# Optimization experiments

Measured on AMD Instinct MI355X. Metric: run time of the kernel, lower is better.

The kernel has to match this reference:

```python
import jax, jax.numpy as jnp
import numpy as np

EMB = 512
HEADS = 8
HEAD_DIM = EMB // HEADS


def setup_inputs() -> dict:
    key = jax.random.key(0)
    ks = jax.random.split(key, 6)
    b, t = 2, 4096
    x = jax.random.normal(ks[0], (b, t, EMB), dtype=jnp.float32)
    sc = 1.0 / np.sqrt(HEAD_DIM).astype(np.float32)
    Wq = jax.random.normal(ks[1], (HEAD_DIM, HEAD_DIM), dtype=jnp.float32) * sc
    Wk = jax.random.normal(ks[2], (HEAD_DIM, HEAD_DIM), dtype=jnp.float32) * sc
    Wv = jax.random.normal(ks[3], (HEAD_DIM, HEAD_DIM), dtype=jnp.float32) * sc
    Wu = jax.random.normal(ks[4], (EMB, EMB), dtype=jnp.float32) * (1.0 / np.sqrt(EMB).astype(np.float32))
    bu = jnp.zeros((EMB,), dtype=jnp.float32)
    return {"x": x, "Wq": Wq, "Wk": Wk, "Wv": Wv, "Wu": Wu, "bu": bu}


def reference(x, Wq, Wk, Wv, Wu, bu):
    b, t, e = x.shape
    s = Wq.shape[0]
    h = e // s
    xh = x.reshape(b, t, h, s)
    # torch Linear: y = x @ W.T (no bias for q/k/v)
    q = jnp.einsum('bthd,ed->bthe', xh, Wq)  # e here == s (head dim)
    k = jnp.einsum('bthd,ed->bthe', xh, Wk)
    v = jnp.einsum('bthd,ed->bthe', xh, Wv)
    # full [b,h,t,t] score matrix, scaled by sqrt(emb_dim) as in source
    dot = jnp.einsum('bqhd,bkhd->bhqk', q, k) / (e ** 0.5)
    att = jax.nn.softmax(dot, axis=-1)
    out = jnp.einsum('bhqk,bkhd->bqhd', att, v).reshape(b, t, e)
    return out @ Wu.T + bu
```

## Files before the change

### kernel.cpp

```cpp
#include <hip/hip_runtime.h>
#include <hip/hip_bf16.h>


#define T 4096
#define HEADS 8
#define HD 64
#define EMB 512
#define BATCH 2
#define BH (BATCH * HEADS)

typedef __attribute__((ext_vector_type(8))) short short8;
typedef __attribute__((ext_vector_type(4))) float floatx4;

__device__ inline short f2bf(float f) {
  union { float f; unsigned u; } v; v.f = f;
  unsigned r = v.u + 0x7FFF + ((v.u >> 16) & 1);
  return (short)(r >> 16);
}

__device__ inline short8 pack8(float4 a, float4 b) {
  short8 o;
  o[0] = f2bf(a.x); o[1] = f2bf(a.y); o[2] = f2bf(a.z); o[3] = f2bf(a.w);
  o[4] = f2bf(b.x); o[5] = f2bf(b.y); o[6] = f2bf(b.z); o[7] = f2bf(b.w);
  return o;
}

__device__ inline short8 packbf(float p0, float p1, float p2, float p3,
                                float p4, float p5, float p6, float p7) {
  union { __hip_bfloat162 h[4]; short8 s; } u;
  float2 t;
  t.x = p0; t.y = p1; u.h[0] = __float22bfloat162_rn(t);
  t.x = p2; t.y = p3; u.h[1] = __float22bfloat162_rn(t);
  t.x = p4; t.y = p5; u.h[2] = __float22bfloat162_rn(t);
  t.x = p6; t.y = p7; u.h[3] = __float22bfloat162_rn(t);
  return u.s;
}

__device__ inline int swz(int row, int byte) {
  return (row * 128 + byte) ^ ((row & 7) << 4);
}

__global__ __launch_bounds__(256) void qkv_kernel(
    const float* __restrict__ x, const float* __restrict__ Wq,
    const float* __restrict__ Wk, const float* __restrict__ Wv,
    short* __restrict__ q_ws, short* __restrict__ k_ws, short* __restrict__ vt_ws) {
  __shared__ __align__(16) short xs[256 * 64];
  const int tid = threadIdx.x;
  const int lane = tid & 63;
  const int w = tid >> 6;
  const int g = lane >> 4, lr = lane & 15;
  const long rowbase = (long)blockIdx.x * 256;

  {
    const float4* xv = (const float4*)(x + (rowbase + tid) * 64);
    for (int c = 0; c < 8; ++c) {
      float4 a = xv[2 * c], b = xv[2 * c + 1];
      *(short8*)((char*)xs + swz(tid, c * 16)) = pack8(a, b);
    }
  }
  __syncthreads();

  const float* Ws[3] = {Wq, Wk, Wv};
  for (int m = 0; m < 3; ++m) {
    const float* W = Ws[m];
    for (int nt = 0; nt < 4; ++nt) {
      const int coln = nt * 16 + lr;
      const float4* wr0 = (const float4*)(W + coln * 64 + 8 * g);
      const float4* wr1 = (const float4*)(W + coln * 64 + 32 + 8 * g);
      short8 b0 = pack8(wr0[0], wr0[1]);
      short8 b1 = pack8(wr1[0], wr1[1]);
      for (int mr = 0; mr < 4; ++mr) {
        const int arow = w * 64 + mr * 16 + lr;
        short8 a0 = *(short8*)((char*)xs + swz(arow, g * 16));
        short8 a1 = *(short8*)((char*)xs + swz(arow, 64 + g * 16));
        floatx4 acc = 0;
        acc = __builtin_amdgcn_mfma_f32_16x16x32_bf16(a0, b0, acc, 0, 0, 0);
        acc = __builtin_amdgcn_mfma_f32_16x16x32_bf16(a1, b1, acc, 0, 0, 0);
        for (int jj = 0; jj < 4; ++jj) {
          long R = rowbase + w * 64 + mr * 16 + 4 * g + jj;
          int bb = (int)(R >> 15);
          int h = (int)(R & 7);
          int t = (int)((R >> 3) & 4095);
          if (m == 0)
            q_ws[(((long)(bb * HEADS + h) * T + t) * 64) + coln] = f2bf(acc[jj]);
          else if (m == 1)
            k_ws[(((long)(bb * HEADS + h) * T + t) * 64) + coln] = f2bf(acc[jj]);
          else {
            int tp = (t & ~31) | (((t >> 2) & 3) << 3) | (((t >> 4) & 1) << 2) | (t & 3);
            vt_ws[((long)(bb * HEADS + h) * 64 + coln) * T + tp] = f2bf(acc[jj]);
          }
        }
      }
    }
  }
}

__global__ __launch_bounds__(256) void attn_kernel(
    const short* __restrict__ q_ws, const short* __restrict__ k_ws,
    const short* __restrict__ vt_ws, short* __restrict__ o_ws) {
  __shared__ __align__(16) short Ks[2][64 * 64];
  __shared__ __align__(16) short Vs[2][64 * 64];
  const int tid = threadIdx.x, lane = tid & 63, w = tid >> 6;
  const int g = lane >> 4, lr = lane & 15;
  const int bh = blockIdx.y;
  const int q0 = blockIdx.x * 128;
  const short* Qp = q_ws + (long)bh * T * 64;
  const short* Kp = k_ws + (long)bh * T * 64;
  const short* Vt = vt_ws + (long)bh * 64 * T;

  const float c2 = 0.0441941738241592f * 1.4426950408889634f;

  short8 aq[2][2];
#pragma unroll
  for (int mt = 0; mt < 2; ++mt) {
    int r = q0 + w * 32 + mt * 16 + lr;
    aq[mt][0] = *(const short8*)(Qp + (long)r * 64 + g * 8);
    aq[mt][1] = *(const short8*)(Qp + (long)r * 64 + 32 + g * 8);
  }

  floatx4 acc[2][4];
#pragma unroll
  for (int mt = 0; mt < 2; ++mt)
#pragma unroll
    for (int dt = 0; dt < 4; ++dt) acc[mt][dt] = 0;
  float ellp[2] = {0.f, 0.f};

  const int srow = tid >> 2;
  const int sseg = (tid & 3) * 16;

  {
    const short8* ksrc = (const short8*)(Kp + (long)srow * 64 + sseg);
    short8 k0 = ksrc[0], k1 = ksrc[1];
    const short8* vsrc = (const short8*)(Vt + (long)srow * T + sseg);
    short8 v0 = vsrc[0], v1 = vsrc[1];
    *(short8*)((char*)Ks[0] + swz(srow, sseg * 2)) = k0;
    *(short8*)((char*)Ks[0] + swz(srow, sseg * 2 + 16)) = k1;
    *(short8*)((char*)Vs[0] + swz(srow, sseg * 2)) = v0;
    *(short8*)((char*)Vs[0] + swz(srow, sseg * 2 + 16)) = v1;
  }
  __syncthreads();

  for (int it = 0; it < T / 64; ++it) {
    const int cur = it & 1;
    const int nk = ((it + 1) & (T / 64 - 1)) * 64;
    const short8* ksrc = (const short8*)(Kp + (long)(nk + srow) * 64 + sseg);
    short8 nk0 = ksrc[0], nk1 = ksrc[1];
    const short8* vsrc = (const short8*)(Vt + (long)srow * T + nk + sseg);
    short8 nv0 = vsrc[0], nv1 = vsrc[1];

    char* KsB = (char*)Ks[cur];
    char* VsB = (char*)Vs[cur];

    short8 kb[4][2], vb[4][2];
#pragma unroll
    for (int kt = 0; kt < 4; ++kt) {
      kb[kt][0] = *(short8*)(KsB + swz(kt * 16 + lr, g * 16));
      kb[kt][1] = *(short8*)(KsB + swz(kt * 16 + lr, 64 + g * 16));
    }
#pragma unroll
    for (int dt = 0; dt < 4; ++dt) {
      vb[dt][0] = *(short8*)(VsB + swz(dt * 16 + lr, g * 16));
      vb[dt][1] = *(short8*)(VsB + swz(dt * 16 + lr, 64 + g * 16));
    }

#pragma unroll
    for (int mt = 0; mt < 2; ++mt) {
      floatx4 s[4];
#pragma unroll
      for (int kt = 0; kt < 4; ++kt) {
        floatx4 z = 0;
        z = __builtin_amdgcn_mfma_f32_16x16x32_bf16(kb[kt][0], aq[mt][0], z, 0, 0, 0);
        z = __builtin_amdgcn_mfma_f32_16x16x32_bf16(kb[kt][1], aq[mt][1], z, 0, 0, 0);
        s[kt] = z;
      }
      float p[16];
#pragma unroll
      for (int kt = 0; kt < 4; ++kt) {
#pragma unroll
        for (int r = 0; r < 4; ++r)
          p[kt * 4 + r] = __builtin_amdgcn_exp2f(fmaf(s[kt][r], c2, -3.0f));
      }
#pragma unroll
      for (int e = 0; e < 16; ++e) ellp[mt] += p[e];
      short8 pa0 = packbf(p[0], p[1], p[2], p[3], p[4], p[5], p[6], p[7]);
      short8 pa1 = packbf(p[8], p[9], p[10], p[11], p[12], p[13], p[14], p[15]);
#pragma unroll
      for (int dt = 0; dt < 4; ++dt) {
        acc[mt][dt] = __builtin_amdgcn_mfma_f32_16x16x32_bf16(pa0, vb[dt][0], acc[mt][dt], 0, 0, 0);
        acc[mt][dt] = __builtin_amdgcn_mfma_f32_16x16x32_bf16(pa1, vb[dt][1], acc[mt][dt], 0, 0, 0);
      }
    }

    char* KsN = (char*)Ks[cur ^ 1];
    char* VsN = (char*)Vs[cur ^ 1];
    *(short8*)(KsN + swz(srow, sseg * 2)) = nk0;
    *(short8*)(KsN + swz(srow, sseg * 2 + 16)) = nk1;
    *(short8*)(VsN + swz(srow, sseg * 2)) = nv0;
    *(short8*)(VsN + swz(srow, sseg * 2 + 16)) = nv1;
    __syncthreads();
  }

  float ef[2];
#pragma unroll
  for (int mt = 0; mt < 2; ++mt) {
    float e = ellp[mt];
    e += __shfl_xor(e, 16);
    e += __shfl_xor(e, 32);
    ef[mt] = e;
  }
  const int bb = bh >> 3, h = bh & 7;
#pragma unroll
  for (int mt = 0; mt < 2; ++mt) {
#pragma unroll
    for (int j = 0; j < 4; ++j) {
      float rl = 1.0f / __shfl(ef[mt], 4 * g + j);
      int trow = q0 + w * 32 + mt * 16 + 4 * g + j;
      long ob = ((long)(bb * T + trow)) * EMB + h * 64;
#pragma unroll
      for (int dt = 0; dt < 4; ++dt)
        o_ws[ob + dt * 16 + lr] = f2bf(acc[mt][dt][j] * rl);
    }
  }
}

__global__ __launch_bounds__(256) void proj_kernel(
    const short* __restrict__ o_ws, const float* __restrict__ Wu,
    const float* __restrict__ bu, float* __restrict__ out) {
  __shared__ __align__(16) short As[64 * 64];
  __shared__ __align__(16) short Bs[64 * 64];
  const int tid = threadIdx.x;
  const int lane = tid & 63, w = tid >> 6;
  const int g = lane >> 4, lr = lane & 15;
  const int m0 = blockIdx.x * 64;
  const int n0 = blockIdx.y * 64;

  floatx4 acc[4];
  for (int nt = 0; nt < 4; ++nt) acc[nt] = 0;

  for (int kc = 0; kc < EMB; kc += 64) {
    {
      int row = tid >> 2, kp = (tid & 3) * 16;
      const short8* src = (const short8*)(o_ws + (long)(m0 + row) * EMB + kc + kp);
      short8 v0 = src[0], v1 = src[1];
      *(short8*)((char*)As + swz(row, kp * 2)) = v0;
      *(short8*)((char*)As + swz(row, kp * 2 + 16)) = v1;
    }
    {
      int n = tid >> 2, kp = (tid & 3) * 16;
      const float4* src = (const float4*)(Wu + (long)(n0 + n) * EMB + kc + kp);
      *(short8*)((char*)Bs + swz(n, kp * 2)) = pack8(src[0], src[1]);
      *(short8*)((char*)Bs + swz(n, kp * 2 + 16)) = pack8(src[2], src[3]);
    }
    __syncthreads();

    int arow = w * 16 + lr;
    short8 a0 = *(short8*)((char*)As + swz(arow, g * 16));
    short8 a1 = *(short8*)((char*)As + swz(arow, 64 + g * 16));
    for (int nt = 0; nt < 4; ++nt) {
      int n = nt * 16 + lr;
      short8 b0 = *(short8*)((char*)Bs + swz(n, g * 16));
      short8 b1 = *(short8*)((char*)Bs + swz(n, 64 + g * 16));
      acc[nt] = __builtin_amdgcn_mfma_f32_16x16x32_bf16(a0, b0, acc[nt], 0, 0, 0);
      acc[nt] = __builtin_amdgcn_mfma_f32_16x16x32_bf16(a1, b1, acc[nt], 0, 0, 0);
    }
    __syncthreads();
  }

  for (int nt = 0; nt < 4; ++nt) {
    float bias = bu[n0 + nt * 16 + lr];
    for (int j = 0; j < 4; ++j) {
      int mrow = m0 + w * 16 + 4 * g + j;
      out[(long)mrow * EMB + n0 + nt * 16 + lr] = acc[nt][j] + bias;
    }
  }
}

extern "C" void kernel_launch(void* const* d_in, const int* in_sizes, int n_in,
                              void* d_out, int out_size, void* d_ws, size_t ws_size,
                              hipStream_t stream) {
  const float* x  = (const float*)d_in[0];
  const float* Wq = (const float*)d_in[1];
  const float* Wk = (const float*)d_in[2];
  const float* Wv = (const float*)d_in[3];
  const float* Wu = (const float*)d_in[4];
  const float* bu = (const float*)d_in[5];
  float* out = (float*)d_out;

  const long per = (long)BH * T * 64;
  short* q_ws  = (short*)d_ws;
  short* k_ws  = q_ws + per;
  short* vt_ws = k_ws + per;
  short* o_ws  = vt_ws + per;

  qkv_kernel<<<256, 256, 0, stream>>>(x, Wq, Wk, Wv, q_ws, k_ws, vt_ws);
  attn_kernel<<<dim3(T / 128, BH), 256, 0, stream>>>(q_ws, k_ws, vt_ws, o_ws);
  proj_kernel<<<dim3(BATCH * T / 64, EMB / 64), 256, 0, stream>>>(o_ws, Wu, bu, out);
}
```

Baseline: 132.2 us.

## Software-pipeline attention loop so PV MFMAs overlap next tile's QK and softmax

```diff
diff --git a/kernel.cpp b/kernel.cpp
--- a/kernel.cpp
+++ b/kernel.cpp
@@ -8,6 +8,7 @@
 #define EMB 512
 #define BATCH 2
 #define BH (BATCH * HEADS)
+#define NT (T / 64)
 
 typedef __attribute__((ext_vector_type(8))) short short8;
 typedef __attribute__((ext_vector_type(4))) float floatx4;
@@ -25,14 +26,13 @@
   return o;
 }
 
-__device__ inline short8 packbf(float p0, float p1, float p2, float p3,
-                                float p4, float p5, float p6, float p7) {
+__device__ inline short8 packbf(const float* p) {
   union { __hip_bfloat162 h[4]; short8 s; } u;
   float2 t;
-  t.x = p0; t.y = p1; u.h[0] = __float22bfloat162_rn(t);
-  t.x = p2; t.y = p3; u.h[1] = __float22bfloat162_rn(t);
-  t.x = p4; t.y = p5; u.h[2] = __float22bfloat162_rn(t);
-  t.x = p6; t.y = p7; u.h[3] = __float22bfloat162_rn(t);
+  t.x = p[0]; t.y = p[1]; u.h[0] = __float22bfloat162_rn(t);
+  t.x = p[2]; t.y = p[3]; u.h[1] = __float22bfloat162_rn(t);
+  t.x = p[4]; t.y = p[5]; u.h[2] = __float22bfloat162_rn(t);
+  t.x = p[6]; t.y = p[7]; u.h[3] = __float22bfloat162_rn(t);
   return u.s;
 }
 
@@ -95,6 +95,56 @@
   }
 }
 
+__device__ __forceinline__ void frag_loads(const char* KsB, const char* VsB,
+    int lr, int g, short8 kb[4][2], short8 vb[4][2]) {
+#pragma unroll
+  for (int kt = 0; kt < 4; ++kt) {
+    kb[kt][0] = *(const short8*)(KsB + swz(kt * 16 + lr, g * 16));
+    kb[kt][1] = *(const short8*)(KsB + swz(kt * 16 + lr, 64 + g * 16));
+  }
+#pragma unroll
+  for (int dt = 0; dt < 4; ++dt) {
+    vb[dt][0] = *(const short8*)(VsB + swz(dt * 16 + lr, g * 16));
+    vb[dt][1] = *(const short8*)(VsB + swz(dt * 16 + lr, 64 + g * 16));
+  }
+}
+
+__device__ __forceinline__ void qkt_softmax(const short8 kb[4][2],
+    const short8 aq[2][2], float c2, float ellp[2], short8 pa[2][2]) {
+#pragma unroll
+  for (int mt = 0; mt < 2; ++mt) {
+    floatx4 s[4];
+#pragma unroll
+    for (int kt = 0; kt < 4; ++kt) {
+      floatx4 z = 0;
+      z = __builtin_amdgcn_mfma_f32_16x16x32_bf16(kb[kt][0], aq[mt][0], z, 0, 0, 0);
+      z = __builtin_amdgcn_mfma_f32_16x16x32_bf16(kb[kt][1], aq[mt][1], z, 0, 0, 0);
+      s[kt] = z;
+    }
+    float p[16];
+#pragma unroll
+    for (int kt = 0; kt < 4; ++kt)
+#pragma unroll
+      for (int r = 0; r < 4; ++r)
+        p[kt * 4 + r] = __builtin_amdgcn_exp2f(fmaf(s[kt][r], c2, -3.0f));
+#pragma unroll
+    for (int e = 0; e < 16; ++e) ellp[mt] += p[e];
+    pa[mt][0] = packbf(p);
+    pa[mt][1] = packbf(p + 8);
+  }
+}
+
+__device__ __forceinline__ void do_pv(const short8 pa[2][2],
+    const short8 vb[4][2], floatx4 acc[2][4]) {
+#pragma unroll
+  for (int mt = 0; mt < 2; ++mt)
+#pragma unroll
+    for (int dt = 0; dt < 4; ++dt) {
+      acc[mt][dt] = __builtin_amdgcn_mfma_f32_16x16x32_bf16(pa[mt][0], vb[dt][0], acc[mt][dt], 0, 0, 0);
+      acc[mt][dt] = __builtin_amdgcn_mfma_f32_16x16x32_bf16(pa[mt][1], vb[dt][1], acc[mt][dt], 0, 0, 0);
+    }
+}
+
 __global__ __launch_bounds__(256) void attn_kernel(
     const short* __restrict__ q_ws, const short* __restrict__ k_ws,
     const short* __restrict__ vt_ws, short* __restrict__ o_ws) {
@@ -128,6 +178,8 @@
   const int srow = tid >> 2;
   const int sseg = (tid & 3) * 16;
 
+  short8 paA[2][2], paB[2][2], vbA[4][2], vbB[4][2];
+
   {
     const short8* ksrc = (const short8*)(Kp + (long)srow * 64 + sseg);
     short8 k0 = ksrc[0], k1 = ksrc[1];
@@ -140,65 +192,36 @@
   }
   __syncthreads();
 
-  for (int it = 0; it < T / 64; ++it) {
-    const int cur = it & 1;
-    const int nk = ((it + 1) & (T / 64 - 1)) * 64;
-    const short8* ksrc = (const short8*)(Kp + (long)(nk + srow) * 64 + sseg);
-    short8 nk0 = ksrc[0], nk1 = ksrc[1];
-    const short8* vsrc = (const short8*)(Vt + (long)srow * T + nk + sseg);
-    short8 nv0 = vsrc[0], nv1 = vsrc[1];
-
-    char* KsB = (char*)Ks[cur];
-    char* VsB = (char*)Vs[cur];
-
-    short8 kb[4][2], vb[4][2];
-#pragma unroll
-    for (int kt = 0; kt < 4; ++kt) {
-      kb[kt][0] = *(short8*)(KsB + swz(kt * 16 + lr, g * 16));
-      kb[kt][1] = *(short8*)(KsB + swz(kt * 16 + lr, 64 + g * 16));
-    }
-#pragma unroll
-    for (int dt = 0; dt < 4; ++dt) {
-      vb[dt][0] = *(short8*)(VsB + swz(dt * 16 + lr, g * 16));
-      vb[dt][1] = *(short8*)(VsB + swz(dt * 16 + lr, 64 + g * 16));
-    }
-
-#pragma unroll
-    for (int mt = 0; mt < 2; ++mt) {
-      floatx4 s[4];
-#pragma unroll
-      for (int kt = 0; kt < 4; ++kt) {
-        floatx4 z = 0;
-        z = __builtin_amdgcn_mfma_f32_16x16x32_bf16(kb[kt][0], aq[mt][0], z, 0, 0, 0);
-        z = __builtin_amdgcn_mfma_f32_16x16x32_bf16(kb[kt][1], aq[mt][1], z, 0, 0, 0);
-        s[kt] = z;
-      }
-      float p[16];
-#pragma unroll
-      for (int kt = 0; kt < 4; ++kt) {
-#pragma unroll
-        for (int r = 0; r < 4; ++r)
-          p[kt * 4 + r] = __builtin_amdgcn_exp2f(fmaf(s[kt][r], c2, -3.0f));
-      }
-#pragma unroll
-      for (int e = 0; e < 16; ++e) ellp[mt] += p[e];
-      short8 pa0 = packbf(p[0], p[1], p[2], p[3], p[4], p[5], p[6], p[7]);
-      short8 pa1 = packbf(p[8], p[9], p[10], p[11], p[12], p[13], p[14], p[15]);
-#pragma unroll
-      for (int dt = 0; dt < 4; ++dt) {
-        acc[mt][dt] = __builtin_amdgcn_mfma_f32_16x16x32_bf16(pa0, vb[dt][0], acc[mt][dt], 0, 0, 0);
-        acc[mt][dt] = __builtin_amdgcn_mfma_f32_16x16x32_bf16(pa1, vb[dt][1], acc[mt][dt], 0, 0, 0);
-      }
-    }
-
-    char* KsN = (char*)Ks[cur ^ 1];
-    char* VsN = (char*)Vs[cur ^ 1];
-    *(short8*)(KsN + swz(srow, sseg * 2)) = nk0;
-    *(short8*)(KsN + swz(srow, sseg * 2 + 16)) = nk1;
-    *(short8*)(VsN + swz(srow, sseg * 2)) = nv0;
-    *(short8*)(VsN + swz(srow, sseg * 2 + 16)) = nv1;
-    __syncthreads();
-  }
+#define BODY(IT, paP, vbP, paO, vbO, DO_PV)                                     \
+  {                                                                             \
+    const int nk = (((IT) + 1) & (NT - 1)) * 64;                                \
+    const short8* ksrc = (const short8*)(Kp + (long)(nk + srow) * 64 + sseg);   \
+    short8 nk0 = ksrc[0], nk1 = ksrc[1];                                        \
+    const short8* vsrc = (const short8*)(Vt + (long)srow * T + nk + sseg);      \
+    short8 nv0 = vsrc[0], nv1 = vsrc[1];                                        \
+    const char* KsB = (const char*)Ks[(IT) & 1];                                \
+    const char* VsB = (const char*)Vs[(IT) & 1];                                \
+    short8 kb[4][2];                                                            \
+    frag_loads(KsB, VsB, lr, g, kb, vbO);                                       \
+    qkt_softmax(kb, aq, c2, ellp, paO);                                         \
+    if (DO_PV) do_pv(paP, vbP, acc);                                            \
+    char* KsN = (char*)Ks[((IT) + 1) & 1];                                      \
+    char* VsN = (char*)Vs[((IT) + 1) & 1];                                      \
+    *(short8*)(KsN + swz(srow, sseg * 2)) = nk0;                                \
+    *(short8*)(KsN + swz(srow, sseg * 2 + 16)) = nk1;                           \
+    *(short8*)(VsN + swz(srow, sseg * 2)) = nv0;                                \
+    *(short8*)(VsN + swz(srow, sseg * 2 + 16)) = nv1;                           \
+    __syncthreads();                                                            \
+  }
+
+  BODY(0, paB, vbB, paA, vbA, 0)
+  for (int k = 0; k < NT / 2 - 1; ++k) {
+    BODY(2 * k + 1, paA, vbA, paB, vbB, 1)
+    BODY(2 * k + 2, paB, vbB, paA, vbA, 1)
+  }
+  BODY(NT - 1, paA, vbA, paB, vbB, 1)
+  do_pv(paB, vbB, acc);
+#undef BODY
 
   float ef[2];
 #pragma unroll
```

New measurement: 139.5 us. 5.5% more time.

## Fold softmax scale into Wq, offset into MFMA init, row sums via MFMA

Applied to the files above, without the earlier changes.

```diff
diff --git a/kernel.cpp b/kernel.cpp
--- a/kernel.cpp
+++ b/kernel.cpp
@@ -8,6 +8,7 @@
 #define EMB 512
 #define BATCH 2
 #define BH (BATCH * HEADS)
+#define NT (T / 64)
 
 typedef __attribute__((ext_vector_type(8))) short short8;
 typedef __attribute__((ext_vector_type(4))) float floatx4;
@@ -25,14 +26,13 @@
   return o;
 }
 
-__device__ inline short8 packbf(float p0, float p1, float p2, float p3,
-                                float p4, float p5, float p6, float p7) {
+__device__ inline short8 packbf(const float* p) {
   union { __hip_bfloat162 h[4]; short8 s; } u;
   float2 t;
-  t.x = p0; t.y = p1; u.h[0] = __float22bfloat162_rn(t);
-  t.x = p2; t.y = p3; u.h[1] = __float22bfloat162_rn(t);
-  t.x = p4; t.y = p5; u.h[2] = __float22bfloat162_rn(t);
-  t.x = p6; t.y = p7; u.h[3] = __float22bfloat162_rn(t);
+  t.x = p[0]; t.y = p[1]; u.h[0] = __float22bfloat162_rn(t);
+  t.x = p[2]; t.y = p[3]; u.h[1] = __float22bfloat162_rn(t);
+  t.x = p[4]; t.y = p[5]; u.h[2] = __float22bfloat162_rn(t);
+  t.x = p[6]; t.y = p[7]; u.h[3] = __float22bfloat162_rn(t);
   return u.s;
 }
 
@@ -50,6 +50,7 @@
   const int w = tid >> 6;
   const int g = lane >> 4, lr = lane & 15;
   const long rowbase = (long)blockIdx.x * 256;
+  const float c2 = 0.0441941738241592f * 1.4426950408889634f;
 
   {
     const float4* xv = (const float4*)(x + (rowbase + tid) * 64);
@@ -63,12 +64,18 @@
   const float* Ws[3] = {Wq, Wk, Wv};
   for (int m = 0; m < 3; ++m) {
     const float* W = Ws[m];
+    const float sc = (m == 0) ? c2 : 1.0f;
     for (int nt = 0; nt < 4; ++nt) {
       const int coln = nt * 16 + lr;
       const float4* wr0 = (const float4*)(W + coln * 64 + 8 * g);
       const float4* wr1 = (const float4*)(W + coln * 64 + 32 + 8 * g);
-      short8 b0 = pack8(wr0[0], wr0[1]);
-      short8 b1 = pack8(wr1[0], wr1[1]);
+      float4 w0 = wr0[0], w1 = wr0[1], w2 = wr1[0], w3 = wr1[1];
+      w0.x *= sc; w0.y *= sc; w0.z *= sc; w0.w *= sc;
+      w1.x *= sc; w1.y *= sc; w1.z *= sc; w1.w *= sc;
+      w2.x *= sc; w2.y *= sc; w2.z *= sc; w2.w *= sc;
+      w3.x *= sc; w3.y *= sc; w3.z *= sc; w3.w *= sc;
+      short8 b0 = pack8(w0, w1);
+      short8 b1 = pack8(w2, w3);
       for (int mr = 0; mr < 4; ++mr) {
         const int arow = w * 64 + mr * 16 + lr;
         short8 a0 = *(short8*)((char*)xs + swz(arow, g * 16));
@@ -108,8 +115,6 @@
   const short* Kp = k_ws + (long)bh * T * 64;
   const short* Vt = vt_ws + (long)bh * 64 * T;
 
-  const float c2 = 0.0441941738241592f * 1.4426950408889634f;
-
   short8 aq[2][2];
 #pragma unroll
   for (int mt = 0; mt < 2; ++mt) {
@@ -118,12 +123,18 @@
     aq[mt][1] = *(const short8*)(Qp + (long)r * 64 + 32 + g * 8);
   }
 
+  short8 one8;
+#pragma unroll
+  for (int e = 0; e < 8; ++e) one8[e] = (short)0x3F80;
+
   floatx4 acc[2][4];
-#pragma unroll
-  for (int mt = 0; mt < 2; ++mt)
+  floatx4 acc_ell[2];
+#pragma unroll
+  for (int mt = 0; mt < 2; ++mt) {
+    acc_ell[mt] = 0;
 #pragma unroll
     for (int dt = 0; dt < 4; ++dt) acc[mt][dt] = 0;
-  float ellp[2] = {0.f, 0.f};
+  }
 
   const int srow = tid >> 2;
   const int sseg = (tid & 3) * 16;
@@ -140,55 +151,58 @@
   }
   __syncthreads();
 
-  for (int it = 0; it < T / 64; ++it) {
+  for (int it = 0; it < NT; ++it) {
     const int cur = it & 1;
-    const int nk = ((it + 1) & (T / 64 - 1)) * 64;
+    const int nk = ((it + 1) & (NT - 1)) * 64;
     const short8* ksrc = (const short8*)(Kp + (long)(nk + srow) * 64 + sseg);
     short8 nk0 = ksrc[0], nk1 = ksrc[1];
     const short8* vsrc = (const short8*)(Vt + (long)srow * T + nk + sseg);
     short8 nv0 = vsrc[0], nv1 = vsrc[1];
 
-    char* KsB = (char*)Ks[cur];
-    char* VsB = (char*)Vs[cur];
+    const char* KsB = (const char*)Ks[cur];
+    const char* VsB = (const char*)Vs[cur];
 
     short8 kb[4][2], vb[4][2];
 #pragma unroll
     for (int kt = 0; kt < 4; ++kt) {
-      kb[kt][0] = *(short8*)(KsB + swz(kt * 16 + lr, g * 16));
-      kb[kt][1] = *(short8*)(KsB + swz(kt * 16 + lr, 64 + g * 16));
+      kb[kt][0] = *(const short8*)(KsB + swz(kt * 16 + lr, g * 16));
+      kb[kt][1] = *(const short8*)(KsB + swz(kt * 16 + lr, 64 + g * 16));
     }
 #pragma unroll
     for (int dt = 0; dt < 4; ++dt) {
-      vb[dt][0] = *(short8*)(VsB + swz(dt * 16 + lr, g * 16));
-      vb[dt][1] = *(short8*)(VsB + swz(dt * 16 + lr, 64 + g * 16));
+      vb[dt][0] = *(const short8*)(VsB + swz(dt * 16 + lr, g * 16));
+      vb[dt][1] = *(const short8*)(VsB + swz(dt * 16 + lr, 64 + g * 16));
     }
 
 #pragma unroll
     for (int mt = 0; mt < 2; ++mt) {
       floatx4 s[4];
+      __builtin_amdgcn_s_setprio(1);
 #pragma unroll
       for (int kt = 0; kt < 4; ++kt) {
-        floatx4 z = 0;
+        floatx4 z = {-3.f, -3.f, -3.f, -3.f};
         z = __builtin_amdgcn_mfma_f32_16x16x32_bf16(kb[kt][0], aq[mt][0], z, 0, 0, 0);
         z = __builtin_amdgcn_mfma_f32_16x16x32_bf16(kb[kt][1], aq[mt][1], z, 0, 0, 0);
         s[kt] = z;
       }
+      __builtin_amdgcn_s_setprio(0);
       float p[16];
 #pragma unroll
-      for (int kt = 0; kt < 4; ++kt) {
+      for (int kt = 0; kt < 4; ++kt)
 #pragma unroll
         for (int r = 0; r < 4; ++r)
-          p[kt * 4 + r] = __builtin_amdgcn_exp2f(fmaf(s[kt][r], c2, -3.0f));
-      }
-#pragma unroll
-      for (int e = 0; e < 16; ++e) ellp[mt] += p[e];
-      short8 pa0 = packbf(p[0], p[1], p[2], p[3], p[4], p[5], p[6], p[7]);
-      short8 pa1 = packbf(p[8], p[9], p[10], p[11], p[12], p[13], p[14], p[15]);
+          p[kt * 4 + r] = __builtin_amdgcn_exp2f(s[kt][r]);
+      short8 pa0 = packbf(p);
+      short8 pa1 = packbf(p + 8);
+      __builtin_amdgcn_s_setprio(1);
 #pragma unroll
       for (int dt = 0; dt < 4; ++dt) {
         acc[mt][dt] = __builtin_amdgcn_mfma_f32_16x16x32_bf16(pa0, vb[dt][0], acc[mt][dt], 0, 0, 0);
         acc[mt][dt] = __builtin_amdgcn_mfma_f32_16x16x32_bf16(pa1, vb[dt][1], acc[mt][dt], 0, 0, 0);
       }
+      acc_ell[mt] = __builtin_amdgcn_mfma_f32_16x16x32_bf16(pa0, one8, acc_ell[mt], 0, 0, 0);
+      acc_ell[mt] = __builtin_amdgcn_mfma_f32_16x16x32_bf16(pa1, one8, acc_ell[mt], 0, 0, 0);
+      __builtin_amdgcn_s_setprio(0);
     }
 
     char* KsN = (char*)Ks[cur ^ 1];
@@ -200,20 +214,12 @@
     __syncthreads();
   }
 
-  float ef[2];
+  const int bb = bh >> 3, h = bh & 7;
 #pragma unroll
   for (int mt = 0; mt < 2; ++mt) {
-    float e = ellp[mt];
-    e += __shfl_xor(e, 16);
-    e += __shfl_xor(e, 32);
-    ef[mt] = e;
-  }
-  const int bb = bh >> 3, h = bh & 7;
-#pragma unroll
-  for (int mt = 0; mt < 2; ++mt) {
 #pragma unroll
     for (int j = 0; j < 4; ++j) {
-      float rl = 1.0f / __shfl(ef[mt], 4 * g + j);
+      float rl = 1.0f / acc_ell[mt][j];
       int trow = q0 + w * 32 + mt * 16 + 4 * g + j;
       long ob = ((long)(bb * T + trow)) * EMB + h * 64;
 #pragma unroll
```

Measured after the change: 140.8 us. 6.5% more time.
